# Optimization experiments

Measured on AMD Instinct MI355X. Metric: run time of the kernel, lower is better.

Reference implementation:

```python
import jax, jax.numpy as jnp
import numpy as np

B, T, D, H, DFF = 2, 2048, 1024, 16, 4096
DK = D // H
EPS = 1e-12
NEG = -1e9

def _ln(x, g, b):
    m = jnp.mean(x, axis=-1, keepdims=True)
    v = jnp.mean((x - m) ** 2, axis=-1, keepdims=True)
    return (x - m) / jnp.sqrt(v + EPS) * g + b

def setup_inputs() -> dict:
    key = jax.random.key(0)
    ks = jax.random.split(key, 8)
    s = 0.02
    return {
        "x": jax.random.normal(ks[0], (B, T, D), jnp.float32),
        "mask": jnp.ones((1, 1, T, T), jnp.int32),
        "wq": jax.random.normal(ks[1], (D, D), jnp.float32) * s,
        "bq": jnp.zeros((D,), jnp.float32),
        "wk": jax.random.normal(ks[2], (D, D), jnp.float32) * s,
        "bk": jnp.zeros((D,), jnp.float32),
        "wv": jax.random.normal(ks[3], (D, D), jnp.float32) * s,
        "bv": jnp.zeros((D,), jnp.float32),
        "wo": jax.random.normal(ks[4], (D, D), jnp.float32) * s,
        "bo": jnp.zeros((D,), jnp.float32),
        "w1": jax.random.normal(ks[5], (DFF, D), jnp.float32) * s,
        "b1": jnp.zeros((DFF,), jnp.float32),
        "w2": jax.random.normal(ks[6], (D, DFF), jnp.float32) * s,
        "b2": jnp.zeros((D,), jnp.float32),
        "g1": jnp.ones((D,), jnp.float32),
        "beta1": jnp.zeros((D,), jnp.float32),
        "g2": jnp.ones((D,), jnp.float32),
        "beta2": jnp.zeros((D,), jnp.float32),
    }

def reference(x, mask, wq, bq, wk, bk, wv, bv, wo, bo, w1, b1, w2, b2, g1, beta1, g2, beta2):
    # pre-norm (note: residual taken from ln1 output, faithful to source)
    xn = _ln(x, g1, beta1)
    # torch Linear: y = x @ W.T + b
    def proj(w, b):
        return (jnp.einsum('btd,ed->bte', xn, w) + b).reshape(B, T, H, DK).transpose(0, 2, 1, 3)
    q = proj(wq, bq)  # [B,H,T,DK]
    k = proj(wk, bk)
    v = proj(wv, bv)
    scores = jnp.einsum('bhqd,bhkd->bhqk', q, k) / jnp.sqrt(jnp.float32(DK))
    scores = jnp.where(mask == 0, jnp.float32(NEG), scores)
    weights = jax.nn.softmax(scores, axis=-1)  # dropout is identity in eval
    att = jnp.einsum('bhqk,bhkd->bhqd', weights, v)
    att = att.transpose(0, 2, 1, 3).reshape(B, T, D)
    h = jnp.einsum('btd,ed->bte', att, wo) + bo
    x = xn + h
    x = _ln(x, g2, beta2)
    ff = jax.nn.relu(jnp.einsum('btd,fd->btf', x, w1) + b1)
    ff = jnp.einsum('btf,df->btd', ff, w2) + b2
    return x + ff
```

## Files before the change

kernel.cpp:

```cpp
#include <hip/hip_runtime.h>

typedef unsigned short u16;
typedef __attribute__((ext_vector_type(8))) short short8;
typedef __attribute__((ext_vector_type(4))) float f32x4;
typedef __attribute__((ext_vector_type(4))) unsigned short u16x4;
typedef __attribute__((ext_vector_type(2))) unsigned int u32x2;

#define DEV static __device__ __forceinline__

DEV u16 f2b(float f) {
    unsigned int u = __builtin_bit_cast(unsigned int, f);
    u += 0x7FFFu + ((u >> 16) & 1u);
    return (u16)(u >> 16);
}
DEV float b2f(u16 v) {
    unsigned int u = ((unsigned int)v) << 16;
    return __builtin_bit_cast(float, u);
}
DEV void gload16(const void* g, void* l) {
    __builtin_amdgcn_global_load_lds((const __attribute__((address_space(1))) void*)g,
                                     (__attribute__((address_space(3))) void*)l,
                                     16, 0, 0);
}
DEV unsigned int cvt_pk(float lo, float hi) {
    unsigned int r;
    asm("v_cvt_pk_bf16_f32 %0, %1, %2" : "=v"(r) : "v"(lo), "v"(hi));
    return r;
}
#if __has_builtin(__builtin_amdgcn_exp2f)
DEV float ex2(float x) { return __builtin_amdgcn_exp2f(x); }
#else
DEV float ex2(float x) { return exp2f(x); }
#endif

static constexpr float KSCALE = 0.18033688011112042f;

__global__ __launch_bounds__(256) void cvt_all_k(
    const float* __restrict__ wq, const float* __restrict__ wk,
    const float* __restrict__ wv, const float* __restrict__ wo,
    const float* __restrict__ w1, const float* __restrict__ w2,
    u16* __restrict__ wqkv, u16* __restrict__ wo_b,
    u16* __restrict__ w1_b, u16* __restrict__ w2_b) {
    int bid = blockIdx.x;
    const float* s; u16* d; int off;
    if (bid < 1024)      { s = wq; d = wqkv;              off = bid; }
    else if (bid < 2048) { s = wk; d = wqkv + 1024*1024;  off = bid - 1024; }
    else if (bid < 3072) { s = wv; d = wqkv + 2048*1024;  off = bid - 2048; }
    else if (bid < 4096) { s = wo; d = wo_b;              off = bid - 3072; }
    else if (bid < 8192) { s = w1; d = w1_b;              off = bid - 4096; }
    else                 { s = w2; d = w2_b;              off = bid - 8192; }
    int i = off * 256 + threadIdx.x;
    float4 v = ((const float4*)s)[i];
    u16x4 o;
    o[0] = f2b(v.x); o[1] = f2b(v.y); o[2] = f2b(v.z); o[3] = f2b(v.w);
    ((u16x4*)d)[i] = o;
}

template <int INTYPE>
__global__ __launch_bounds__(256) void ln_k(const void* __restrict__ in,
                                            const float* __restrict__ g,
                                            const float* __restrict__ be,
                                            u16* __restrict__ outb) {
    int row = blockIdx.x;
    int t = threadIdx.x;
    float v[4];
    if constexpr (INTYPE == 0) {
        float4 x = ((const float4*)((const float*)in + (size_t)row * 1024))[t];
        v[0] = x.x; v[1] = x.y; v[2] = x.z; v[3] = x.w;
    } else {
        u16x4 x = ((const u16x4*)((const u16*)in + (size_t)row * 1024))[t];
#pragma unroll
        for (int i = 0; i < 4; i++) v[i] = b2f(x[i]);
    }
    float s = v[0] + v[1] + v[2] + v[3];
    float s2 = v[0] * v[0] + v[1] * v[1] + v[2] * v[2] + v[3] * v[3];
#pragma unroll
    for (int off = 1; off < 64; off <<= 1) {
        s += __shfl_xor(s, off);
        s2 += __shfl_xor(s2, off);
    }
    __shared__ float red[8];
    int wid = t >> 6, lane = t & 63;
    if (lane == 0) { red[wid] = s; red[4 + wid] = s2; }
    __syncthreads();
    float S = red[0] + red[1] + red[2] + red[3];
    float S2 = red[4] + red[5] + red[6] + red[7];
    float mean = S * (1.f / 1024.f);
    float var = fmaxf(S2 * (1.f / 1024.f) - mean * mean, 0.f);
    float rinv = rsqrtf(var + 1e-12f);
    float4 gv = ((const float4*)g)[t];
    float4 bv = ((const float4*)be)[t];
    u16x4 o;
    o[0] = f2b((v[0] - mean) * rinv * gv.x + bv.x);
    o[1] = f2b((v[1] - mean) * rinv * gv.y + bv.y);
    o[2] = f2b((v[2] - mean) * rinv * gv.z + bv.z);
    o[3] = f2b((v[3] - mean) * rinv * gv.w + bv.w);
    ((u16x4*)(outb + (size_t)row * 1024))[t] = o;
}

template <int EPI>
__global__ __launch_bounds__(512, 2) void gemm256(
    const u16* __restrict__ A, const u16* __restrict__ Bw,
    const float* __restrict__ b0, const float* __restrict__ b1,
    const float* __restrict__ b2, u16* __restrict__ outb,
    u16* __restrict__ kb, u16* __restrict__ vb, int M, int N, int K) {
    __shared__ u16 SB[3 * 16384];
    int tid = threadIdx.x, wid = tid >> 6, lane = tid & 63;
    int l15 = lane & 15, l4 = lane >> 4;
    int m0 = blockIdx.y * 256, n0 = blockIdx.x * 256;
    int wr = wid >> 2, wc = wid & 3;

    f32x4 acc[8][4] = {};

    int srow = tid >> 2;
    int sc = (tid & 3) * 8;
    const u16* Ag  = A  + (size_t)(m0 + srow) * K + sc;
    const u16* Ag2 = Ag + (size_t)128 * K;
    const u16* Bg  = Bw + (size_t)(n0 + srow) * K + sc;
    const u16* Bg2 = Bg + (size_t)128 * K;
    int ldst = wid * 1024;

    auto stageA = [&](int t, int bufi) {
        char* base = (char*)SB + bufi * 32768;
        size_t ko = (size_t)t * 32;
        gload16(Ag + ko, base + ldst);
        gload16(Ag2 + ko, base + 8192 + ldst);
    };
    auto stageB = [&](int t, int bufi) {
        char* base = (char*)SB + bufi * 32768 + 16384;
        size_t ko = (size_t)t * 32;
        gload16(Bg + ko, base + ldst);
        gload16(Bg2 + ko, base + 8192 + ldst);
    };

    const int NT = K >> 5;
    stageA(0, 0); stageB(0, 0);
    stageA(1, 1); stageB(1, 1);

    int cb = 0;
    for (int i = 0; i < NT; ++i) {
        if (i == NT - 1) asm volatile("s_waitcnt vmcnt(0)" ::: "memory");
        else             asm volatile("s_waitcnt vmcnt(4)" ::: "memory");
        __builtin_amdgcn_s_barrier();
        __builtin_amdgcn_sched_barrier(0);
        int sb = cb + 2; if (sb >= 3) sb -= 3;

        const u16* Abuf = SB + cb * 16384;
        const u16* Bbuf = Abuf + 8192;
        const u16* ap = &Abuf[(wr * 128 + l15) * 32 + l4 * 8];
        const u16* bp = &Bbuf[(wc * 64 + l15) * 32 + l4 * 8];
        short8 af[8], bfr[4];
#pragma unroll
        for (int x = 0; x < 4; x++) {
            af[x]  = *(const short8*)(ap + x * 512);
            bfr[x] = *(const short8*)(bp + x * 512);
        }
        if (i + 2 < NT) stageA(i + 2, sb);
#pragma unroll
        for (int x = 4; x < 8; x++) af[x] = *(const short8*)(ap + x * 512);
        if (i + 2 < NT) stageB(i + 2, sb);
        __builtin_amdgcn_s_setprio(1);
#pragma unroll
        for (int mi = 0; mi < 8; mi++)
#pragma unroll
            for (int ni = 0; ni < 4; ni++)
                acc[mi][ni] = __builtin_amdgcn_mfma_f32_16x16x32_bf16(
                    af[mi], bfr[ni], acc[mi][ni], 0, 0, 0);
        __builtin_amdgcn_s_setprio(0);
        cb = (cb == 2) ? 0 : cb + 1;
    }

#pragma unroll
    for (int mi = 0; mi < 8; mi++) {
#pragma unroll
        for (int ni = 0; ni < 4; ni++) {
            int n = n0 + wc * 64 + ni * 16 + l15;
            int mr = m0 + wr * 128 + mi * 16 + l4 * 4;
            if constexpr (EPI == 0) {
                int bidx = m0 >> 11;
                int t = mr & 2047;
                if (n0 < 1024) {
                    float bias = b0[n];
#pragma unroll
                    for (int r = 0; r < 4; r++)
                        outb[(size_t)(mr + r) * 1024 + n] =
                            f2b(acc[mi][ni][r] + bias);
                } else if (n0 < 2048) {
                    int nk = n - 1024, hh = nk >> 6, dk = nk & 63;
                    float bias = b1[nk];
                    size_t base = ((size_t)(bidx * 16 + hh) * 2048 + t) * 64 + dk;
#pragma unroll
                    for (int r = 0; r < 4; r++)
                        kb[base + (size_t)r * 64] =
                            f2b((acc[mi][ni][r] + bias) * KSCALE);
                } else {
                    int nv = n - 2048, hh = nv >> 6, dk = nv & 63;
                    int tile = t >> 5, kv = t & 31;
                    float bias = b2[nv];
                    u16x4 pk;
#pragma unroll
                    for (int r = 0; r < 4; r++) pk[r] = f2b(acc[mi][ni][r] + bias);
                    *(u16x4*)&vb[((((size_t)(bidx * 16 + hh) * 64 + tile) * 64 +
                                   dk) << 5) + kv] = pk;
                }
            } else {
                float bias = b0[n];
#pragma unroll
                for (int r = 0; r < 4; r++)
                    outb[(size_t)(mr + r) * N + n] =
                        f2b(fmaxf(acc[mi][ni][r] + bias, 0.f));
            }
        }
    }
}

template <int EPI, int BM>
__global__ __launch_bounds__(256) void gemm_bt(
    const u16* __restrict__ A, const u16* __restrict__ Bw,
    const float* __restrict__ b0, u16* __restrict__ outb,
    float* __restrict__ outf, const u16* __restrict__ res,
    int M, int N, int K) {
    constexpr int MFR = BM / 32;
    constexpr int BS = (BM + 128) * 32;
    __shared__ u16 SB[3 * BS];
    int tid = threadIdx.x, wid = tid >> 6, lane = tid & 63;
    int l15 = lane & 15, l4 = lane >> 4;
    int m0 = blockIdx.y * BM, n0 = blockIdx.x * 128;
    int wr = wid >> 1, wc = wid & 1;

    f32x4 acc[MFR][4] = {};

    int srow = tid >> 2;
    int scol = (tid & 3) * 8;
    const u16* Ag  = A  + (size_t)(m0 + srow) * K + scol;
    const u16* Ag2 = Ag + (size_t)64 * K;
    const u16* Bg  = Bw + (size_t)(n0 + srow) * K + scol;
    const u16* Bg2 = Bg + (size_t)64 * K;
    int ldst = wid * 1024;

    auto stage = [&](int t, int bufi) {
        char* base = (char*)SB + (size_t)bufi * (BS * 2);
        size_t ko = (size_t)t * 32;
        gload16(Ag + ko, base + ldst);
        if constexpr (BM == 128) gload16(Ag2 + ko, base + 4096 + ldst);
        gload16(Bg + ko, base + BM * 64 + ldst);
        gload16(Bg2 + ko, base + BM * 64 + 4096 + ldst);
    };

    const int NT = K >> 5;
    stage(0, 0);
    stage(1, 1);

    int cb = 0;
    for (int i = 0; i < NT; ++i) {
        if (i == NT - 1) {
            asm volatile("s_waitcnt vmcnt(0)" ::: "memory");
        } else if constexpr (BM == 128) {
            asm volatile("s_waitcnt vmcnt(4)" ::: "memory");
        } else {
            asm volatile("s_waitcnt vmcnt(3)" ::: "memory");
        }
        __builtin_amdgcn_s_barrier();
        __builtin_amdgcn_sched_barrier(0);
        int sb = cb + 2; if (sb >= 3) sb -= 3;
        if (i + 2 < NT) stage(i + 2, sb);

        const u16* Abuf = SB + (size_t)cb * BS;
        const u16* Bbuf = Abuf + BM * 32;
        short8 af[MFR], bfr[4];
        const u16* ap = &Abuf[(wr * (BM / 2) + l15) * 32 + l4 * 8];
        const u16* bp = &Bbuf[(wc * 64 + l15) * 32 + l4 * 8];
#pragma unroll
        for (int i2 = 0; i2 < MFR; i2++) af[i2] = *(const short8*)(ap + i2 * 512);
#pragma unroll
        for (int i2 = 0; i2 < 4; i2++) bfr[i2] = *(const short8*)(bp + i2 * 512);
#pragma unroll
        for (int mi = 0; mi < MFR; mi++)
#pragma unroll
            for (int ni = 0; ni < 4; ni++)
                acc[mi][ni] = __builtin_amdgcn_mfma_f32_16x16x32_bf16(
                    af[mi], bfr[ni], acc[mi][ni], 0, 0, 0);
        cb = (cb == 2) ? 0 : cb + 1;
    }

    int mbase = m0 + wr * (BM / 2);
    int nbase = n0 + wc * 64;
#pragma unroll
    for (int mi = 0; mi < MFR; mi++) {
#pragma unroll
        for (int ni = 0; ni < 4; ni++) {
            int n = nbase + ni * 16 + l15;
            int mr = mbase + mi * 16 + l4 * 4;
            float bias = b0[n];
            if constexpr (EPI == 1) {
#pragma unroll
                for (int i = 0; i < 4; i++) {
                    size_t off = (size_t)(mr + i) * N + n;
                    outb[off] = f2b(acc[mi][ni][i] + bias + b2f(res[off]));
                }
            } else {
#pragma unroll
                for (int i = 0; i < 4; i++) {
                    size_t off = (size_t)(mr + i) * N + n;
                    outf[off] = acc[mi][ni][i] + bias + b2f(res[off]);
                }
            }
        }
    }
}

#define ATT_STAGE(KN, VN, TILE) do {                                          \
    int tl_ = ((TILE) + phase) & 31;                                          \
    gload16(Kg + tl_ * 2048, (char*)(KN) + ldst);                             \
    gload16(Vg + tl_ * 2048, (char*)(VN) + ldst);                             \
} while (0)

#define ATT_COMPUTE(KL, VL) do {                                              \
    f32x4 s_acc[2][2] = {};                                                   \
    {                                                                         \
        short8 kf[2][2];                                                      \
        _Pragma("unroll")                                                     \
        for (int kvt = 0; kvt < 2; kvt++) {                                   \
            int row = kvt * 16 + l15;                                         \
            kf[kvt][0] = *(const short8*)&(KL)[row * 64 + ((l4) ^ (row & 7)) * 8]; \
            kf[kvt][1] = *(const short8*)&(KL)[row * 64 + ((4 + l4) ^ (row & 7)) * 8]; \
        }                                                                     \
        __builtin_amdgcn_s_setprio(1);                                        \
        _Pragma("unroll")                                                     \
        for (int kvt = 0; kvt < 2; kvt++)                                     \
            _Pragma("unroll")                                                 \
            for (int qfi = 0; qfi < 2; qfi++) {                               \
                s_acc[kvt][qfi] = __builtin_amdgcn_mfma_f32_16x16x32_bf16(    \
                    kf[kvt][0], qf[qfi][0], s_acc[kvt][qfi], 0, 0, 0);        \
                s_acc[kvt][qfi] = __builtin_amdgcn_mfma_f32_16x16x32_bf16(    \
                    kf[kvt][1], qf[qfi][1], s_acc[kvt][qfi], 0, 0, 0);        \
            }                                                                 \
        __builtin_amdgcn_s_setprio(0);                                        \
    }                                                                         \
    _Pragma("unroll")                                                         \
    for (int qfi = 0; qfi < 2; qfi++) {                                       \
        char* Pq = Pw + qfi * 1152;                                           \
        _Pragma("unroll")                                                     \
        for (int kvt = 0; kvt < 2; kvt++) {                                   \
            u32x2 w;                                                          \
            w[0] = cvt_pk(ex2(s_acc[kvt][qfi][0]), ex2(s_acc[kvt][qfi][1]));  \
            w[1] = cvt_pk(ex2(s_acc[kvt][qfi][2]), ex2(s_acc[kvt][qfi][3]));  \
            *(u32x2*)(Pq + l15 * 72 + kvt * 32 + l4 * 8) = w;                 \
        }                                                                     \
    }                                                                         \
    {                                                                         \
        short8 pf[2], vf[4];                                                  \
        _Pragma("unroll")                                                     \
        for (int qfi = 0; qfi < 2; qfi++)                                     \
            pf[qfi] = *(const short8*)(Pw + qfi * 1152 + l15 * 72 + l4 * 16); \
        _Pragma("unroll")                                                     \
        for (int dt = 0; dt < 4; dt++) {                                      \
            int row = dt * 16 + l15;                                          \
            vf[dt] = *(const short8*)&(VL)[row * 32 + ((l4 ^ ((row >> 1) & 3))) * 8]; \
        }                                                                     \
        __builtin_amdgcn_s_setprio(1);                                        \
        _Pragma("unroll")                                                     \
        for (int qfi = 0; qfi < 2; qfi++)                                     \
            o_sum[qfi] = __builtin_amdgcn_mfma_f32_16x16x32_bf16(             \
                ones, pf[qfi], o_sum[qfi], 0, 0, 0);                          \
        _Pragma("unroll")                                                     \
        for (int dt = 0; dt < 4; dt++)                                        \
            _Pragma("unroll")                                                 \
            for (int qfi = 0; qfi < 2; qfi++)                                 \
                o_acc[dt][qfi] = __builtin_amdgcn_mfma_f32_16x16x32_bf16(     \
                    vf[dt], pf[qfi], o_acc[dt][qfi], 0, 0, 0);                \
        __builtin_amdgcn_s_setprio(0);                                        \
    }                                                                         \
} while (0)

#define ATT_ITER(CK, CV, NK, NV, TILE) do {                                   \
    asm volatile("s_waitcnt vmcnt(2)" ::: "memory");                          \
    __builtin_amdgcn_s_barrier();                                             \
    __builtin_amdgcn_sched_barrier(0);                                        \
    ATT_STAGE(NK, NV, TILE);                                                  \
    ATT_COMPUTE(CK, CV);                                                      \
} while (0)

__global__ __launch_bounds__(256, 4) void attn_k(const u16* __restrict__ qb,
                                                 const u16* __restrict__ kb,
                                                 const u16* __restrict__ vb,
                                                 u16* __restrict__ p0,
                                                 u16* __restrict__ p1,
                                                 float* __restrict__ s0,
                                                 float* __restrict__ s1) {
    __shared__ u16 K_lds[3][32 * 64];
    __shared__ u16 V_lds[3][64 * 32];
    __shared__ u16 P_lds[4][2][16 * 36];
    int tid = threadIdx.x, wid = tid >> 6, lane = tid & 63;
    int l15 = lane & 15, l4 = lane >> 4;
    int bh = blockIdx.y, b = bh >> 4, h = bh & 15;
    int z = blockIdx.z;
    size_t boff = (size_t)b * 2048;
    int q0 = blockIdx.x * 128 + wid * 32;
    int phase = (blockIdx.x * 5 + blockIdx.y * 3 + blockIdx.z * 11) & 31;

    short8 qf[2][2];
#pragma unroll
    for (int qfi = 0; qfi < 2; qfi++) {
        const u16* qrow = qb + (boff + q0 + qfi * 16 + l15) * 1024 + h * 64 + l4 * 8;
        qf[qfi][0] = *(const short8*)(qrow);
        qf[qfi][1] = *(const short8*)(qrow + 32);
    }
    short8 ones;
#pragma unroll
    for (int j = 0; j < 8; j++) ones[j] = (short)0x3F80;

    f32x4 o_acc[4][2] = {};
    f32x4 o_sum[2] = {};
    char* Pw = (char*)&P_lds[wid][0][0];

    int krow = tid >> 3, kcs = (tid & 7) ^ (krow & 7);
    const u16* Kg = kb + ((size_t)bh * 2048 + z * 1024) * 64 + krow * 64 + kcs * 8;
    int vrow = tid >> 2, vcs = (tid & 3) ^ ((vrow >> 1) & 3);
    const u16* Vg = vb + ((size_t)bh * 64 + z * 32) * 2048 + vrow * 32 + vcs * 8;
    int ldst = wid * 1024;

    ATT_STAGE(&K_lds[0][0], &V_lds[0][0], 0);
    ATT_STAGE(&K_lds[1][0], &V_lds[1][0], 1);
    for (int g = 0; g < 10; g++) {
        ATT_ITER(&K_lds[0][0], &V_lds[0][0], &K_lds[2][0], &V_lds[2][0], 3 * g + 2);
        ATT_ITER(&K_lds[1][0], &V_lds[1][0], &K_lds[0][0], &V_lds[0][0], 3 * g + 3);
        ATT_ITER(&K_lds[2][0], &V_lds[2][0], &K_lds[1][0], &V_lds[1][0], 3 * g + 4);
    }
    asm volatile("s_waitcnt vmcnt(2)" ::: "memory");
    __builtin_amdgcn_s_barrier();
    __builtin_amdgcn_sched_barrier(0);
    ATT_COMPUTE(&K_lds[0][0], &V_lds[0][0]);
    asm volatile("s_waitcnt vmcnt(0)" ::: "memory");
    __builtin_amdgcn_s_barrier();
    __builtin_amdgcn_sched_barrier(0);
    ATT_COMPUTE(&K_lds[1][0], &V_lds[1][0]);

    u16* pz = z ? p1 : p0;
    float* sz = z ? s1 : s0;
#pragma unroll
    for (int qfi = 0; qfi < 2; qfi++) {
        int q = q0 + qfi * 16 + l15;
#pragma unroll
        for (int dt = 0; dt < 4; dt++) {
            u16x4 o;
#pragma unroll
            for (int r = 0; r < 4; r++) o[r] = f2b(o_acc[dt][qfi][r]);
            *(u16x4*)&pz[(boff + q) * 1024 + h * 64 + dt * 16 + l4 * 4] = o;
        }
        if (l4 == 0) sz[(boff + q) * 16 + h] = o_sum[qfi][0];
    }
}

__global__ __launch_bounds__(256) void attn_cmb(
    const u16* __restrict__ p0, const u16* __restrict__ p1,
    const float* __restrict__ s0, const float* __restrict__ s1,
    u16* __restrict__ att) {
    int idx = blockIdx.x * 256 + threadIdx.x;
    int row = idx >> 7, oct = idx & 127;
    int h = oct >> 3;
    float rs = 1.f / (s0[row * 16 + h] + s1[row * 16 + h]);
    size_t off = (size_t)row * 1024 + oct * 8;
    u16x4 a0 = ((const u16x4*)(p0 + off))[0];
    u16x4 a1 = ((const u16x4*)(p0 + off))[1];
    u16x4 c0 = ((const u16x4*)(p1 + off))[0];
    u16x4 c1 = ((const u16x4*)(p1 + off))[1];
    u16x4 o0, o1;
#pragma unroll
    for (int j = 0; j < 4; j++) {
        o0[j] = f2b((b2f(a0[j]) + b2f(c0[j])) * rs);
        o1[j] = f2b((b2f(a1[j]) + b2f(c1[j])) * rs);
    }
    ((u16x4*)(att + off))[0] = o0;
    ((u16x4*)(att + off))[1] = o1;
}

extern "C" void kernel_launch(void* const* d_in, const int* in_sizes, int n_in,
                              void* d_out, int out_size, void* d_ws, size_t ws_size,
                              hipStream_t stream) {
    (void)in_sizes; (void)n_in; (void)out_size; (void)ws_size;
    const float* x   = (const float*)d_in[0];
    const float* wq  = (const float*)d_in[2];
    const float* bq  = (const float*)d_in[3];
    const float* wk  = (const float*)d_in[4];
    const float* bk  = (const float*)d_in[5];
    const float* wv  = (const float*)d_in[6];
    const float* bv  = (const float*)d_in[7];
    const float* wo  = (const float*)d_in[8];
    const float* bo  = (const float*)d_in[9];
    const float* w1  = (const float*)d_in[10];
    const float* b1  = (const float*)d_in[11];
    const float* w2  = (const float*)d_in[12];
    const float* b2  = (const float*)d_in[13];
    const float* g1  = (const float*)d_in[14];
    const float* be1 = (const float*)d_in[15];
    const float* g2  = (const float*)d_in[16];
    const float* be2 = (const float*)d_in[17];
    float* out = (float*)d_out;

    char* ws = (char*)d_ws;
    u16* wqkv  = (u16*)(ws + (size_t)0);
    u16* wo_b  = (u16*)(ws + ((size_t)6  << 20));
    u16* w1_b  = (u16*)(ws + ((size_t)8  << 20));
    u16* w2_b  = (u16*)(ws + ((size_t)16 << 20));
    u16* xn_b  = (u16*)(ws + ((size_t)24 << 20));
    u16* x2_b  = (u16*)(ws + ((size_t)32 << 20));
    u16* x3_b  = (u16*)(ws + ((size_t)40 << 20));
    u16* q_b   = (u16*)(ws + ((size_t)48 << 20));
    u16* k_b   = (u16*)(ws + ((size_t)56 << 20));
    u16* v_b   = (u16*)(ws + ((size_t)64 << 20));
    u16* att_b = (u16*)(ws + ((size_t)72 << 20));
    float* s0_b = (float*)(ws + ((size_t)80 << 20));
    float* s1_b = (float*)(ws + ((size_t)80 << 20) + 262144);
    u16* ff_b  = (u16*)(ws + ((size_t)48 << 20));

    cvt_all_k<<<12288, 256, 0, stream>>>(wq, wk, wv, wo, w1, w2,
                                         wqkv, wo_b, w1_b, w2_b);
    ln_k<0><<<4096, 256, 0, stream>>>(x, g1, be1, xn_b);
    gemm256<0><<<dim3(12, 16), 512, 0, stream>>>(
        xn_b, wqkv, bq, bk, bv, q_b, k_b, v_b, 4096, 3072, 1024);
    attn_k<<<dim3(16, 32, 2), 256, 0, stream>>>(q_b, k_b, v_b, x2_b, x3_b,
                                                s0_b, s1_b);
    attn_cmb<<<2048, 256, 0, stream>>>(x2_b, x3_b, s0_b, s1_b, att_b);
    gemm_bt<1, 64><<<dim3(8, 64), 256, 0, stream>>>(
        att_b, wo_b, bo, x2_b, nullptr, xn_b, 4096, 1024, 1024);
    ln_k<1><<<4096, 256, 0, stream>>>(x2_b, g2, be2, x3_b);
    gemm256<2><<<dim3(16, 16), 512, 0, stream>>>(
        x3_b, w1_b, b1, nullptr, nullptr, ff_b, nullptr, nullptr, 4096, 4096, 1024);
    gemm_bt<3, 64><<<dim3(8, 64), 256, 0, stream>>>(
        ff_b, w2_b, b2, nullptr, out, x3_b, 4096, 1024, 4096);
}
```

Before: 242.2 us.

## Split attention KV across waves in-block and fuse combine into kernel

Restructures the attention kernel so that each block covers 32 queries, and its four waves each handle a quarter of the key/value sequence from private double-buffered LDS tiles with no block barriers. The partial outputs and softmax sums are then reduced through shared memory inside the block, which removes the separate combine kernel and the bf16 partial-output round trip to global memory. Block indices are remapped so that blocks sharing a head land on the same XCD, aiming for better L2 reuse of K/V. In exchange, each wave loads K/V only for its own 32 queries, so the per-query K/V traffic rises, LDS use per block grows, and occupancy drops to 2 blocks per CU.

Result: slower. 250.8 us (+3.6%).

```diff
diff --git a/kernel.cpp b/kernel.cpp
--- a/kernel.cpp
+++ b/kernel.cpp
@@ -309,100 +309,25 @@
     }
 }
 
-#define ATT_STAGE(KN, VN, TILE) do {                                          \
-    int tl_ = ((TILE) + phase) & 31;                                          \
-    gload16(Kg + tl_ * 2048, (char*)(KN) + ldst);                             \
-    gload16(Vg + tl_ * 2048, (char*)(VN) + ldst);                             \
-} while (0)
-
-#define ATT_COMPUTE(KL, VL) do {                                              \
-    f32x4 s_acc[2][2] = {};                                                   \
-    {                                                                         \
-        short8 kf[2][2];                                                      \
-        _Pragma("unroll")                                                     \
-        for (int kvt = 0; kvt < 2; kvt++) {                                   \
-            int row = kvt * 16 + l15;                                         \
-            kf[kvt][0] = *(const short8*)&(KL)[row * 64 + ((l4) ^ (row & 7)) * 8]; \
-            kf[kvt][1] = *(const short8*)&(KL)[row * 64 + ((4 + l4) ^ (row & 7)) * 8]; \
-        }                                                                     \
-        __builtin_amdgcn_s_setprio(1);                                        \
-        _Pragma("unroll")                                                     \
-        for (int kvt = 0; kvt < 2; kvt++)                                     \
-            _Pragma("unroll")                                                 \
-            for (int qfi = 0; qfi < 2; qfi++) {                               \
-                s_acc[kvt][qfi] = __builtin_amdgcn_mfma_f32_16x16x32_bf16(    \
-                    kf[kvt][0], qf[qfi][0], s_acc[kvt][qfi], 0, 0, 0);        \
-                s_acc[kvt][qfi] = __builtin_amdgcn_mfma_f32_16x16x32_bf16(    \
-                    kf[kvt][1], qf[qfi][1], s_acc[kvt][qfi], 0, 0, 0);        \
-            }                                                                 \
-        __builtin_amdgcn_s_setprio(0);                                        \
-    }                                                                         \
-    _Pragma("unroll")                                                         \
-    for (int qfi = 0; qfi < 2; qfi++) {                                       \
-        char* Pq = Pw + qfi * 1152;                                           \
-        _Pragma("unroll")                                                     \
-        for (int kvt = 0; kvt < 2; kvt++) {                                   \
-            u32x2 w;                                                          \
-            w[0] = cvt_pk(ex2(s_acc[kvt][qfi][0]), ex2(s_acc[kvt][qfi][1]));  \
-            w[1] = cvt_pk(ex2(s_acc[kvt][qfi][2]), ex2(s_acc[kvt][qfi][3]));  \
-            *(u32x2*)(Pq + l15 * 72 + kvt * 32 + l4 * 8) = w;                 \
-        }                                                                     \
-    }                                                                         \
-    {                                                                         \
-        short8 pf[2], vf[4];                                                  \
-        _Pragma("unroll")                                                     \
-        for (int qfi = 0; qfi < 2; qfi++)                                     \
-            pf[qfi] = *(const short8*)(Pw + qfi * 1152 + l15 * 72 + l4 * 16); \
-        _Pragma("unroll")                                                     \
-        for (int dt = 0; dt < 4; dt++) {                                      \
-            int row = dt * 16 + l15;                                          \
-            vf[dt] = *(const short8*)&(VL)[row * 32 + ((l4 ^ ((row >> 1) & 3))) * 8]; \
-        }                                                                     \
-        __builtin_amdgcn_s_setprio(1);                                        \
-        _Pragma("unroll")                                                     \
-        for (int qfi = 0; qfi < 2; qfi++)                                     \
-            o_sum[qfi] = __builtin_amdgcn_mfma_f32_16x16x32_bf16(             \
-                ones, pf[qfi], o_sum[qfi], 0, 0, 0);                          \
-        _Pragma("unroll")                                                     \
-        for (int dt = 0; dt < 4; dt++)                                        \
-            _Pragma("unroll")                                                 \
-            for (int qfi = 0; qfi < 2; qfi++)                                 \
-                o_acc[dt][qfi] = __builtin_amdgcn_mfma_f32_16x16x32_bf16(     \
-                    vf[dt], pf[qfi], o_acc[dt][qfi], 0, 0, 0);                \
-        __builtin_amdgcn_s_setprio(0);                                        \
-    }                                                                         \
-} while (0)
-
-#define ATT_ITER(CK, CV, NK, NV, TILE) do {                                   \
-    asm volatile("s_waitcnt vmcnt(2)" ::: "memory");                          \
-    __builtin_amdgcn_s_barrier();                                             \
-    __builtin_amdgcn_sched_barrier(0);                                        \
-    ATT_STAGE(NK, NV, TILE);                                                  \
-    ATT_COMPUTE(CK, CV);                                                      \
-} while (0)
-
-__global__ __launch_bounds__(256, 4) void attn_k(const u16* __restrict__ qb,
+__global__ __launch_bounds__(256, 2) void attn_k(const u16* __restrict__ qb,
                                                  const u16* __restrict__ kb,
                                                  const u16* __restrict__ vb,
-                                                 u16* __restrict__ p0,
-                                                 u16* __restrict__ p1,
-                                                 float* __restrict__ s0,
-                                                 float* __restrict__ s1) {
-    __shared__ u16 K_lds[3][32 * 64];
-    __shared__ u16 V_lds[3][64 * 32];
-    __shared__ u16 P_lds[4][2][16 * 36];
+                                                 u16* __restrict__ att) {
+    __shared__ u16 SM[37376];
     int tid = threadIdx.x, wid = tid >> 6, lane = tid & 63;
     int l15 = lane & 15, l4 = lane >> 4;
-    int bh = blockIdx.y, b = bh >> 4, h = bh & 15;
-    int z = blockIdx.z;
+    int lin = blockIdx.x + 64 * blockIdx.y;
+    int xcd = lin & 7, ii = lin >> 3;
+    int bh = ((ii >> 6) << 3) + xcd;
+    int qblk = ii & 63;
+    int b = bh >> 4, head = bh & 15;
     size_t boff = (size_t)b * 2048;
-    int q0 = blockIdx.x * 128 + wid * 32;
-    int phase = (blockIdx.x * 5 + blockIdx.y * 3 + blockIdx.z * 11) & 31;
+    int q0 = qblk * 32;
 
     short8 qf[2][2];
 #pragma unroll
     for (int qfi = 0; qfi < 2; qfi++) {
-        const u16* qrow = qb + (boff + q0 + qfi * 16 + l15) * 1024 + h * 64 + l4 * 8;
+        const u16* qrow = qb + (boff + q0 + qfi * 16 + l15) * 1024 + head * 64 + l4 * 8;
         qf[qfi][0] = *(const short8*)(qrow);
         qf[qfi][1] = *(const short8*)(qrow + 32);
     }
@@ -412,67 +337,134 @@
 
     f32x4 o_acc[4][2] = {};
     f32x4 o_sum[2] = {};
-    char* Pw = (char*)&P_lds[wid][0][0];
-
-    int krow = tid >> 3, kcs = (tid & 7) ^ (krow & 7);
-    const u16* Kg = kb + ((size_t)bh * 2048 + z * 1024) * 64 + krow * 64 + kcs * 8;
-    int vrow = tid >> 2, vcs = (tid & 3) ^ ((vrow >> 1) & 3);
-    const u16* Vg = vb + ((size_t)bh * 64 + z * 32) * 2048 + vrow * 32 + vcs * 8;
-    int ldst = wid * 1024;
-
-    ATT_STAGE(&K_lds[0][0], &V_lds[0][0], 0);
-    ATT_STAGE(&K_lds[1][0], &V_lds[1][0], 1);
-    for (int g = 0; g < 10; g++) {
-        ATT_ITER(&K_lds[0][0], &V_lds[0][0], &K_lds[2][0], &V_lds[2][0], 3 * g + 2);
-        ATT_ITER(&K_lds[1][0], &V_lds[1][0], &K_lds[0][0], &V_lds[0][0], 3 * g + 3);
-        ATT_ITER(&K_lds[2][0], &V_lds[2][0], &K_lds[1][0], &V_lds[1][0], 3 * g + 4);
-    }
-    asm volatile("s_waitcnt vmcnt(2)" ::: "memory");
-    __builtin_amdgcn_s_barrier();
-    __builtin_amdgcn_sched_barrier(0);
-    ATT_COMPUTE(&K_lds[0][0], &V_lds[0][0]);
-    asm volatile("s_waitcnt vmcnt(0)" ::: "memory");
-    __builtin_amdgcn_s_barrier();
-    __builtin_amdgcn_sched_barrier(0);
-    ATT_COMPUTE(&K_lds[1][0], &V_lds[1][0]);
-
-    u16* pz = z ? p1 : p0;
-    float* sz = z ? s1 : s0;
+
+    u16* K0 = SM + wid * 8192;
+    u16* K1 = K0 + 2048;
+    u16* V0 = K0 + 4096;
+    u16* V1 = K0 + 6144;
+    char* Pw = (char*)(SM + 32768 + wid * 1152);
+
+    const u16* Kt = kb + ((size_t)bh * 2048 + wid * 512) * 64;
+    const u16* Vt = vb + ((size_t)(bh * 64 + wid * 16)) * 2048;
+    int kOff = (lane >> 3) * 64 + (((lane & 7) ^ ((lane >> 3) & 7))) * 8;
+    int vOff = (lane >> 2) * 32 + (((lane & 3) ^ ((lane >> 3) & 3))) * 8;
+
+#define ATT_STG(TILE, KB, VB) do {                                            \
+    size_t o_ = (size_t)(TILE) * 2048;                                        \
+    gload16(Kt + o_ + kOff,        (char*)(KB));                              \
+    gload16(Kt + o_ + 512 + kOff,  (char*)(KB) + 1024);                       \
+    gload16(Kt + o_ + 1024 + kOff, (char*)(KB) + 2048);                       \
+    gload16(Kt + o_ + 1536 + kOff, (char*)(KB) + 3072);                       \
+    gload16(Vt + o_ + vOff,        (char*)(VB));                              \
+    gload16(Vt + o_ + 512 + vOff,  (char*)(VB) + 1024);                       \
+    gload16(Vt + o_ + 1024 + vOff, (char*)(VB) + 2048);                       \
+    gload16(Vt + o_ + 1536 + vOff, (char*)(VB) + 3072);                       \
+} while (0)
+
+    int ph = qblk & 15;
+    ATT_STG((0 + ph) & 15, K0, V0);
+    ATT_STG((1 + ph) & 15, K1, V1);
+
+#pragma unroll
+    for (int t = 0; t < 16; t++) {
+        if (t < 15) asm volatile("s_waitcnt vmcnt(8)" ::: "memory");
+        else        asm volatile("s_waitcnt vmcnt(0)" ::: "memory");
+        u16* KL = (t & 1) ? K1 : K0;
+        u16* VL = (t & 1) ? V1 : V0;
+        short8 kf[2][2], vf[4];
+#pragma unroll
+        for (int kvt = 0; kvt < 2; kvt++) {
+            int row = kvt * 16 + l15;
+            kf[kvt][0] = *(const short8*)&KL[row * 64 + ((l4) ^ (row & 7)) * 8];
+            kf[kvt][1] = *(const short8*)&KL[row * 64 + ((4 + l4) ^ (row & 7)) * 8];
+        }
+#pragma unroll
+        for (int dt = 0; dt < 4; dt++) {
+            int row = dt * 16 + l15;
+            vf[dt] = *(const short8*)&VL[row * 32 + ((l4 ^ ((row >> 1) & 3))) * 8];
+        }
+        asm volatile("s_waitcnt lgkmcnt(0)" ::: "memory");
+        __builtin_amdgcn_sched_barrier(0);
+        if (t + 2 < 16) ATT_STG((t + 2 + ph) & 15, KL, VL);
+        f32x4 s_acc[2][2] = {};
+        __builtin_amdgcn_s_setprio(1);
+#pragma unroll
+        for (int kvt = 0; kvt < 2; kvt++)
+#pragma unroll
+            for (int qfi = 0; qfi < 2; qfi++) {
+                s_acc[kvt][qfi] = __builtin_amdgcn_mfma_f32_16x16x32_bf16(
+                    kf[kvt][0], qf[qfi][0], s_acc[kvt][qfi], 0, 0, 0);
+                s_acc[kvt][qfi] = __builtin_amdgcn_mfma_f32_16x16x32_bf16(
+                    kf[kvt][1], qf[qfi][1], s_acc[kvt][qfi], 0, 0, 0);
+            }
+        __builtin_amdgcn_s_setprio(0);
+#pragma unroll
+        for (int qfi = 0; qfi < 2; qfi++) {
+            char* Pq = Pw + qfi * 1152;
+#pragma unroll
+            for (int kvt = 0; kvt < 2; kvt++) {
+                u32x2 w;
+                w[0] = cvt_pk(ex2(s_acc[kvt][qfi][0]), ex2(s_acc[kvt][qfi][1]));
+                w[1] = cvt_pk(ex2(s_acc[kvt][qfi][2]), ex2(s_acc[kvt][qfi][3]));
+                *(u32x2*)(Pq + l15 * 72 + kvt * 32 + l4 * 8) = w;
+            }
+        }
+        {
+            short8 pf[2];
+#pragma unroll
+            for (int qfi = 0; qfi < 2; qfi++)
+                pf[qfi] = *(const short8*)(Pw + qfi * 1152 + l15 * 72 + l4 * 16);
+            __builtin_amdgcn_s_setprio(1);
+#pragma unroll
+            for (int qfi = 0; qfi < 2; qfi++)
+                o_sum[qfi] = __builtin_amdgcn_mfma_f32_16x16x32_bf16(
+                    ones, pf[qfi], o_sum[qfi], 0, 0, 0);
+#pragma unroll
+            for (int dt = 0; dt < 4; dt++)
+#pragma unroll
+                for (int qfi = 0; qfi < 2; qfi++)
+                    o_acc[dt][qfi] = __builtin_amdgcn_mfma_f32_16x16x32_bf16(
+                        vf[dt], pf[qfi], o_acc[dt][qfi], 0, 0, 0);
+            __builtin_amdgcn_s_setprio(0);
+        }
+    }
+#undef ATT_STG
+
+    __syncthreads();
+    float* ocmb = (float*)SM;
+    float* lcmb = (float*)((char*)SM + 34816);
 #pragma unroll
     for (int qfi = 0; qfi < 2; qfi++) {
-        int q = q0 + qfi * 16 + l15;
-#pragma unroll
-        for (int dt = 0; dt < 4; dt++) {
-            u16x4 o;
-#pragma unroll
-            for (int r = 0; r < 4; r++) o[r] = f2b(o_acc[dt][qfi][r]);
-            *(u16x4*)&pz[(boff + q) * 1024 + h * 64 + dt * 16 + l4 * 4] = o;
-        }
-        if (l4 == 0) sz[(boff + q) * 16 + h] = o_sum[qfi][0];
-    }
-}
-
-__global__ __launch_bounds__(256) void attn_cmb(
-    const u16* __restrict__ p0, const u16* __restrict__ p1,
-    const float* __restrict__ s0, const float* __restrict__ s1,
-    u16* __restrict__ att) {
-    int idx = blockIdx.x * 256 + threadIdx.x;
-    int row = idx >> 7, oct = idx & 127;
-    int h = oct >> 3;
-    float rs = 1.f / (s0[row * 16 + h] + s1[row * 16 + h]);
-    size_t off = (size_t)row * 1024 + oct * 8;
-    u16x4 a0 = ((const u16x4*)(p0 + off))[0];
-    u16x4 a1 = ((const u16x4*)(p0 + off))[1];
-    u16x4 c0 = ((const u16x4*)(p1 + off))[0];
-    u16x4 c1 = ((const u16x4*)(p1 + off))[1];
-    u16x4 o0, o1;
-#pragma unroll
-    for (int j = 0; j < 4; j++) {
-        o0[j] = f2b((b2f(a0[j]) + b2f(c0[j])) * rs);
-        o1[j] = f2b((b2f(a1[j]) + b2f(c1[j])) * rs);
-    }
-    ((u16x4*)(att + off))[0] = o0;
-    ((u16x4*)(att + off))[1] = o1;
+        int ql = qfi * 16 + l15;
+#pragma unroll
+        for (int dt = 0; dt < 4; dt++)
+            *(f32x4*)&ocmb[wid * 2176 + ql * 68 + dt * 16 + l4 * 4] =
+                o_acc[dt][qfi];
+        if (l4 == 0) lcmb[wid * 32 + ql] = o_sum[qfi][0];
+    }
+    __syncthreads();
+    {
+        int q = tid >> 3, oct = tid & 7;
+        float l = lcmb[q] + lcmb[32 + q] + lcmb[64 + q] + lcmb[96 + q];
+        float rl = 1.f / l;
+        int base = q * 68 + oct * 8;
+        f32x4 a0 = *(f32x4*)&ocmb[base];
+        f32x4 a1 = *(f32x4*)&ocmb[base + 4];
+#pragma unroll
+        for (int w = 1; w < 4; w++) {
+            a0 += *(f32x4*)&ocmb[w * 2176 + base];
+            a1 += *(f32x4*)&ocmb[w * 2176 + base + 4];
+        }
+        u16x4 o0, o1;
+#pragma unroll
+        for (int j = 0; j < 4; j++) {
+            o0[j] = f2b(a0[j] * rl);
+            o1[j] = f2b(a1[j] * rl);
+        }
+        u16* orow = att + (boff + q0 + q) * 1024 + head * 64 + oct * 8;
+        ((u16x4*)orow)[0] = o0;
+        ((u16x4*)orow)[1] = o1;
+    }
 }
 
 extern "C" void kernel_launch(void* const* d_in, const int* in_sizes, int n_in,
@@ -510,8 +502,6 @@
     u16* k_b   = (u16*)(ws + ((size_t)56 << 20));
     u16* v_b   = (u16*)(ws + ((size_t)64 << 20));
     u16* att_b = (u16*)(ws + ((size_t)72 << 20));
-    float* s0_b = (float*)(ws + ((size_t)80 << 20));
-    float* s1_b = (float*)(ws + ((size_t)80 << 20) + 262144);
     u16* ff_b  = (u16*)(ws + ((size_t)48 << 20));
 
     cvt_all_k<<<12288, 256, 0, stream>>>(wq, wk, wv, wo, w1, w2,
@@ -519,9 +509,7 @@
     ln_k<0><<<4096, 256, 0, stream>>>(x, g1, be1, xn_b);
     gemm256<0><<<dim3(12, 16), 512, 0, stream>>>(
         xn_b, wqkv, bq, bk, bv, q_b, k_b, v_b, 4096, 3072, 1024);
-    attn_k<<<dim3(16, 32, 2), 256, 0, stream>>>(q_b, k_b, v_b, x2_b, x3_b,
-                                                s0_b, s1_b);
-    attn_cmb<<<2048, 256, 0, stream>>>(x2_b, x3_b, s0_b, s1_b, att_b);
+    attn_k<<<dim3(64, 32), 256, 0, stream>>>(q_b, k_b, v_b, att_b);
     gemm_bt<1, 64><<<dim3(8, 64), 256, 0, stream>>>(
         att_b, wo_b, bo, x2_b, nullptr, xn_b, 4096, 1024, 1024);
     ln_k<1><<<4096, 256, 0, stream>>>(x2_b, g2, be2, x3_b);
```
